# Optimization experiments

Measured on AMD Instinct MI355X. Metric: run time of the kernel, lower is better.

## Reference

```python
import jax, jax.numpy as jnp
import numpy as np

N_NODES = 50000
N_EDGES = 800000
D = 128        # input_dim == output_dim
D_EDGE = 64    # edge_attr_size
Z_DIM = 2 * D + D_EDGE  # 320


def setup_inputs() -> dict:
    key = jax.random.key(0)
    k1, k2, k3, k4, k5 = jax.random.split(key, 5)
    x = jax.random.normal(k1, (N_NODES, D), dtype=jnp.float32)
    edge_index = jax.random.randint(k2, (2, N_EDGES), 0, N_NODES, dtype=jnp.int64)
    edge_attr = jax.random.normal(k3, (N_EDGES, D_EDGE), dtype=jnp.float32)
    scale = 1.0 / np.sqrt(Z_DIM)
    W_f = jax.random.normal(k4, (Z_DIM, D), dtype=jnp.float32) * scale
    W_s = jax.random.normal(k5, (Z_DIM, D), dtype=jnp.float32) * scale
    b_f = jnp.zeros((D,), dtype=jnp.float32)
    b_s = jnp.zeros((D,), dtype=jnp.float32)
    return {"x": x, "edge_index": edge_index, "edge_attr": edge_attr,
            "W_f": W_f, "b_f": b_f, "W_s": W_s, "b_s": b_s}


def reference(x, edge_index, edge_attr, W_f, b_f, W_s, b_s):
    # Dropout(p=0.0) is identity in inference.
    src = edge_index[0]  # j (message source)
    dst = edge_index[1]  # i (message target)
    # z_e = [x_i, x_j, e_ij]  -> [E, 2D + D_edge]
    z = jnp.concatenate([x[dst], x[src], edge_attr], axis=-1)
    # CGConv message: sigmoid(lin_f(z)) * softplus(lin_s(z))
    msg = jax.nn.sigmoid(z @ W_f + b_f) * jax.nn.softplus(z @ W_s + b_s)
    # scatter-add aggregation + residual
    out = jax.ops.segment_sum(msg, dst, num_segments=x.shape[0]) + x
    # use_activation=True -> ReLU
    return jax.nn.relu(out)
```

## Files before the change

kernel.cpp:

```cpp
#include <hip/hip_runtime.h>
#include <hip/hip_bf16.h>

#define E_TOTAL   800000
#define NN        50000
#define DD        128
#define DE        64
#define ZDIM      320
#define KE        192
#define MT        64
#define NBS       196

typedef short bf16x8 __attribute__((ext_vector_type(8)));
typedef float f32x4  __attribute__((ext_vector_type(4)));

__device__ __forceinline__ unsigned short f2bf(float f) {
    union { float f; unsigned int u; } v; v.f = f;
    unsigned int u = v.u;
    return (unsigned short)((u + 0x7fffu + ((u >> 16) & 1u)) >> 16);
}

__device__ __forceinline__ float bf2f(unsigned short h) {
    union { unsigned u; float f; } v; v.u = ((unsigned)h) << 16; return v.f;
}

__device__ __forceinline__ unsigned pkbf2(float a, float b) {
    __hip_bfloat162 h = __float22bfloat162_rn(make_float2(a, b));
    unsigned u; __builtin_memcpy(&u, &h, 4); return u;
}

__device__ __forceinline__ uint2 pkbf4(float4 v) {
    uint2 r; r.x = pkbf2(v.x, v.y); r.y = pkbf2(v.z, v.w); return r;
}

__device__ __forceinline__ float fast_rcp(float x) {
#if __has_builtin(__builtin_amdgcn_rcpf)
    return __builtin_amdgcn_rcpf(x);
#else
    return 1.0f / x;
#endif
}


__global__ void scan_part(const int* __restrict__ counts, int* __restrict__ partial) {
    __shared__ int red[256];
    int t = threadIdx.x, k = blockIdx.x * 256 + t;
    red[t] = (k < NN) ? counts[k] : 0;
    __syncthreads();
    for (int d = 128; d > 0; d >>= 1) {
        if (t < d) red[t] += red[t + d];
        __syncthreads();
    }
    if (t == 0) partial[blockIdx.x] = red[0];
}

__global__ void scan_top(int* __restrict__ partial) {
    __shared__ int s[256];
    int t = threadIdx.x;
    int v = (t < NBS) ? partial[t] : 0;
    s[t] = v; __syncthreads();
    for (int d = 1; d < 256; d <<= 1) {
        int a = (t >= d) ? s[t - d] : 0;
        __syncthreads();
        s[t] += a;
        __syncthreads();
    }
    if (t < NBS) partial[t] = s[t] - v;
}

__global__ void scan_final(const int* __restrict__ counts,
                           const int* __restrict__ partial,
                           int* __restrict__ cursor) {
    __shared__ int s[256];
    int t = threadIdx.x, k = blockIdx.x * 256 + t;
    int v = (k < NN) ? counts[k] : 0;
    s[t] = v; __syncthreads();
    for (int d = 1; d < 256; d <<= 1) {
        int a = (t >= d) ? s[t - d] : 0;
        __syncthreads();
        s[t] += a;
        __syncthreads();
    }
    if (k < NN) cursor[k] = partial[blockIdx.x] + s[t] - v;
}

__global__ void scatter_kernel(const int* __restrict__ ei, int* __restrict__ cursor,
                               uint2* __restrict__ spak2) {
    int e = blockIdx.x * 256 + threadIdx.x;
    if (e < E_TOTAL) {
        int d = ei[E_TOTAL + e];
        int pos = atomicAdd(&cursor[d], 1);
        uint2 p; p.x = ((unsigned)d << 16) | (unsigned)ei[e]; p.y = (unsigned)e;
        spak2[pos] = p;
    }
}


__global__ void prep_kernel2(const float* __restrict__ x,
                             const int* __restrict__ ei,
                             const float* __restrict__ W_f,
                             const float* __restrict__ W_s,
                             unsigned short* __restrict__ WtE,
                             unsigned short* __restrict__ WtN,
                             int* __restrict__ counts,
                             float* __restrict__ out) {
    int id = blockIdx.x * 256 + threadIdx.x;
    ((float4*)out)[id] = ((const float4*)x)[id];
    if (id < E_TOTAL) atomicAdd(&counts[ei[E_TOTAL + id]], 1);
    if (id < 256 * DE) {
        int n = id >> 6, k = id & 63;
        int ok = 2 * DD + k;
        float wv = (n < DD) ? W_f[ok * DD + n] : W_s[ok * DD + (n - DD)];
        WtE[id] = f2bf(wv);
    } else if (id < 256 * DE + 2 * 256 * DD) {
        int id2 = id - 256 * DE;
        int part = id2 >> 15;
        int r = id2 & 32767;
        int n = r >> 7, k = r & 127;
        int ok = part * DD + k;
        float wv = (n < DD) ? W_f[ok * DD + n] : W_s[ok * DD + (n - DD)];
        WtN[id2] = f2bf(wv);
    }
}

__global__ __launch_bounds__(256, 4)
void node_kernel2(const float* __restrict__ x,
                  const unsigned short* __restrict__ WtN,
                  const float* __restrict__ bf_, const float* __restrict__ bs_,
                  unsigned short* __restrict__ nodeP) {
    __shared__ unsigned short A_lds[MT * DD];
    const int t = threadIdx.x;
    const int m_off = blockIdx.x * MT;
    const int part = blockIdx.y;
    const int lane = t & 63, w = t >> 6, l15 = lane & 15, quad = lane >> 4;

    #pragma unroll
    for (int it = 0; it < 8; ++it) {
        int idx = it * 256 + t;
        int e = idx >> 5, kq = idx & 31;
        int row = m_off + e; if (row >= NN) row = NN - 1;
        float4 v = ((const float4*)(x + (size_t)row * DD))[kq];
        int g = kq >> 1;
        int col = ((g & ~7) | ((g & 7) ^ (e & 7))) * 8 + (kq & 1) * 4;
        *((uint2*)&A_lds[e * DD + col]) = pkbf4(v);
    }

    f32x4 acc[4][4] = {};
    const int nt0 = 2 * w;
    const unsigned short* Bp[4];
    #pragma unroll
    for (int u = 0; u < 4; ++u) {
        int nt = nt0 + ((u < 2) ? u : (6 + u));
        Bp[u] = WtN + (size_t)part * (256 * DD) + (size_t)(nt * 16 + l15) * DD + quad * 8;
    }
    __syncthreads();

    #pragma unroll
    for (int ks = 0; ks < 4; ++ks) {
        bf16x8 af[4], bfr[4];
        #pragma unroll
        for (int i = 0; i < 4; ++i) {
            int m = i * 16 + l15;
            int g = 4 * ks + quad;
            int col = ((g & ~7) | ((g & 7) ^ (l15 & 7))) * 8;
            af[i] = *((const bf16x8*)&A_lds[m * DD + col]);
        }
        #pragma unroll
        for (int u = 0; u < 4; ++u)
            bfr[u] = *((const bf16x8*)(Bp[u] + ks * 32));
        #pragma unroll
        for (int i = 0; i < 4; ++i)
            #pragma unroll
            for (int u = 0; u < 4; ++u)
                acc[i][u] = __builtin_amdgcn_mfma_f32_16x16x32_bf16(
                    af[i], bfr[u], acc[i][u], 0, 0, 0);
    }

    const int c0 = 32 * w + l15, c1 = c0 + 16;
    const float bf0 = part ? 0.f : bf_[c0], bs0 = part ? 0.f : bs_[c0];
    const float bf1 = part ? 0.f : bf_[c1], bs1 = part ? 0.f : bs_[c1];
    #pragma unroll
    for (int i = 0; i < 4; ++i)
        #pragma unroll
        for (int j = 0; j < 4; ++j) {
            int e = i * 16 + quad * 4 + j;
            int row = m_off + e;
            if (row < NN) {
                uint2 pk;
                pk.x = pkbf2(acc[i][0][j] + bf0, acc[i][1][j] + bf1);
                pk.y = pkbf2(acc[i][2][j] + bs0, acc[i][3][j] + bs1);
                *((uint2*)(nodeP + (size_t)row * 512 + part * 256 + w * 64 + l15 * 4)) = pk;
            }
        }
}

#define PS_LOAD(PS, I)                                                          \
    _Pragma("unroll")                                                           \
    for (int j = 0; j < 4; ++j)                                                 \
        PS[j] = *((const uint2*)(npS + (size_t)src_lds[(I) * 16 + quad * 4 + j] * 512));

#define PS_PROC(PS, I)                                                          \
    _Pragma("unroll")                                                           \
    for (int j = 0; j < 4; ++j) {                                               \
        int e = (I) * 16 + quad * 4 + j;                                        \
        int dd = dst_lds[e];                                                    \
        if (dd != d) {                                                          \
            if (d >= 0) {                                                       \
                atomicAdd(out + (size_t)d * DD + c0, s0);                       \
                atomicAdd(out + (size_t)d * DD + c1, s1);                       \
            }                                                                   \
            d = dd; s0 = 0.f; s1 = 0.f;                                         \
            uint2 pk = *((const uint2*)(nodeP + (size_t)d * 512 + np_off));     \
            nf0 = bf2f((unsigned short)(pk.x & 0xffffu));                       \
            nf1 = bf2f((unsigned short)(pk.x >> 16));                           \
            ns0 = bf2f((unsigned short)(pk.y & 0xffffu));                       \
            ns1 = bf2f((unsigned short)(pk.y >> 16));                           \
        }                                                                       \
        uint2 pp = PS[j];                                                       \
        float f0  = acc[(I)][0][j] + nf0 + bf2f((unsigned short)(pp.x & 0xffffu)); \
        float f1  = acc[(I)][1][j] + nf1 + bf2f((unsigned short)(pp.x >> 16));  \
        float sg0 = acc[(I)][2][j] + ns0 + bf2f((unsigned short)(pp.y & 0xffffu)); \
        float sg1 = acc[(I)][3][j] + ns1 + bf2f((unsigned short)(pp.y >> 16));  \
        s0 += fast_rcp(1.f + __expf(-f0)) *                                     \
              (fmaxf(sg0, 0.f) + __logf(1.f + __expf(-fabsf(sg0))));            \
        s1 += fast_rcp(1.f + __expf(-f1)) *                                     \
              (fmaxf(sg1, 0.f) + __logf(1.f + __expf(-fabsf(sg1))));            \
    }

__global__ __launch_bounds__(256, 4)
void edge_kernel2(const float* __restrict__ ea,
                  const unsigned short* __restrict__ WtE,
                  const unsigned short* __restrict__ nodeP,
                  float* __restrict__ out,
                  const uint2* __restrict__ spak2) {
    __shared__ unsigned short A_lds[MT * DE];
    __shared__ int dst_lds[MT];
    __shared__ int src_lds[MT];
    __shared__ int eid_lds[MT];

    const int t = threadIdx.x;
    const int m_off = blockIdx.x * MT;
    const int lane = t & 63, w = t >> 6, l15 = lane & 15, quad = lane >> 4;

    if (t < MT) {
        uint2 p = spak2[m_off + t];
        dst_lds[t] = (int)(p.x >> 16);
        src_lds[t] = (int)(p.x & 0xffffu);
        eid_lds[t] = (int)p.y;
    }
    __syncthreads();

    #pragma unroll
    for (int it = 0; it < 4; ++it) {
        int idx = it * 256 + t;
        int e = idx >> 4, kq = idx & 15;
        float4 v = ((const float4*)(ea + (size_t)eid_lds[e] * DE))[kq];
        int g = kq >> 1;
        int col = ((g & 7) ^ (e & 7)) * 8 + (kq & 1) * 4;
        *((uint2*)&A_lds[e * DE + col]) = pkbf4(v);
    }

    f32x4 acc[4][4] = {};
    const int nt0 = 2 * w;
    const unsigned short* Bp[4];
    #pragma unroll
    for (int u = 0; u < 4; ++u) {
        int nt = nt0 + ((u < 2) ? u : (6 + u));
        Bp[u] = WtE + (size_t)(nt * 16 + l15) * DE + quad * 8;
    }
    __syncthreads();

    #pragma unroll
    for (int ks = 0; ks < 2; ++ks) {
        bf16x8 af[4], bfr[4];
        #pragma unroll
        for (int i = 0; i < 4; ++i) {
            int m = i * 16 + l15;
            int g = 4 * ks + quad;
            int col = ((g & 7) ^ (l15 & 7)) * 8;
            af[i] = *((const bf16x8*)&A_lds[m * DE + col]);
        }
        #pragma unroll
        for (int u = 0; u < 4; ++u)
            bfr[u] = *((const bf16x8*)(Bp[u] + ks * 32));
        #pragma unroll
        for (int i = 0; i < 4; ++i)
            #pragma unroll
            for (int u = 0; u < 4; ++u)
                acc[i][u] = __builtin_amdgcn_mfma_f32_16x16x32_bf16(
                    af[i], bfr[u], acc[i][u], 0, 0, 0);
    }

    const int c0 = 32 * w + l15, c1 = c0 + 16;
    const int np_off = w * 64 + l15 * 4;
    const unsigned short* npS = nodeP + 256 + np_off;

    int d = -1;
    float s0 = 0.f, s1 = 0.f, nf0 = 0.f, ns0 = 0.f, nf1 = 0.f, ns1 = 0.f;
    uint2 psA[4], psB[4];
    PS_LOAD(psA, 0)
    PS_LOAD(psB, 1)
    PS_PROC(psA, 0)
    PS_LOAD(psA, 2)
    PS_PROC(psB, 1)
    PS_LOAD(psB, 3)
    PS_PROC(psA, 2)
    PS_PROC(psB, 3)
    atomicAdd(out + (size_t)d * DD + c0, s0);
    atomicAdd(out + (size_t)d * DD + c1, s1);
}


__global__ void prep_kernel(const float* __restrict__ x,
                            const int* __restrict__ ei,
                            const float* __restrict__ W_f,
                            const float* __restrict__ W_s,
                            unsigned short* __restrict__ WtE,
                            unsigned short* __restrict__ WtN,
                            int* __restrict__ counts,
                            float* __restrict__ out) {
    int id = blockIdx.x * 256 + threadIdx.x;
    ((float4*)out)[id] = ((const float4*)x)[id];
    if (id < E_TOTAL) atomicAdd(&counts[ei[E_TOTAL + id]], 1);
    if (id < 256 * KE) {
        int n = id / KE, k = id - n * KE;
        int ok = 128 + k;
        float wv = (n < DD) ? W_f[ok * DD + n] : W_s[ok * DD + (n - DD)];
        WtE[id] = f2bf(wv);
    } else if (id < 256 * KE + 256 * DD) {
        int id2 = id - 256 * KE;
        int n = id2 / DD, k = id2 - n * DD;
        float wv = (n < DD) ? W_f[k * DD + n] : W_s[k * DD + (n - DD)];
        WtN[id2] = f2bf(wv);
    }
}

__global__ __launch_bounds__(256, 4)
void node_kernel(const float* __restrict__ x,
                 const unsigned short* __restrict__ WtN,
                 const float* __restrict__ bf_, const float* __restrict__ bs_,
                 unsigned short* __restrict__ nodeP) {
    __shared__ unsigned short A_lds[MT * DD];
    const int t = threadIdx.x;
    const int m_off = blockIdx.x * MT;
    const int lane = t & 63, w = t >> 6, l15 = lane & 15, quad = lane >> 4;

    #pragma unroll
    for (int it = 0; it < 8; ++it) {
        int idx = it * 256 + t;
        int e = idx >> 5, kq = idx & 31;
        int row = m_off + e; if (row >= NN) row = NN - 1;
        float4 v = ((const float4*)(x + (size_t)row * DD))[kq];
        int g = kq >> 1;
        int col = ((g & ~7) | ((g & 7) ^ (e & 7))) * 8 + (kq & 1) * 4;
        *((uint2*)&A_lds[e * DD + col]) = pkbf4(v);
    }

    f32x4 acc[4][4] = {};
    const int nt0 = 2 * w;
    const unsigned short* Bp[4];
    #pragma unroll
    for (int u = 0; u < 4; ++u) {
        int nt = nt0 + ((u < 2) ? u : (6 + u));
        Bp[u] = WtN + (size_t)(nt * 16 + l15) * DD + quad * 8;
    }
    __syncthreads();

    #pragma unroll
    for (int ks = 0; ks < 4; ++ks) {
        bf16x8 af[4], bfr[4];
        #pragma unroll
        for (int i = 0; i < 4; ++i) {
            int m = i * 16 + l15;
            int g = 4 * ks + quad;
            int col = ((g & ~7) | ((g & 7) ^ (l15 & 7))) * 8;
            af[i] = *((const bf16x8*)&A_lds[m * DD + col]);
        }
        #pragma unroll
        for (int u = 0; u < 4; ++u)
            bfr[u] = *((const bf16x8*)(Bp[u] + ks * 32));
        #pragma unroll
        for (int i = 0; i < 4; ++i)
            #pragma unroll
            for (int u = 0; u < 4; ++u)
                acc[i][u] = __builtin_amdgcn_mfma_f32_16x16x32_bf16(
                    af[i], bfr[u], acc[i][u], 0, 0, 0);
    }

    const int c0 = 32 * w + l15, c1 = c0 + 16;
    const float bf0 = bf_[c0], bs0 = bs_[c0], bf1 = bf_[c1], bs1 = bs_[c1];
    #pragma unroll
    for (int i = 0; i < 4; ++i)
        #pragma unroll
        for (int j = 0; j < 4; ++j) {
            int e = i * 16 + quad * 4 + j;
            int row = m_off + e;
            if (row < NN) {
                uint2 pk;
                pk.x = pkbf2(acc[i][0][j] + bf0, acc[i][1][j] + bf1);
                pk.y = pkbf2(acc[i][2][j] + bs0, acc[i][3][j] + bs1);
                *((uint2*)(nodeP + (size_t)row * 256 + w * 64 + l15 * 4)) = pk;
            }
        }
}

__global__ __launch_bounds__(256, 4)
void edge_kernel(const float* __restrict__ x,
                 const float* __restrict__ ea,
                 const unsigned short* __restrict__ WtE,
                 const unsigned short* __restrict__ nodeP,
                 float* __restrict__ out,
                 const uint2* __restrict__ spak2) {
    __shared__ unsigned short A_lds[MT * KE];
    __shared__ int dst_lds[MT];
    __shared__ int src_lds[MT];
    __shared__ int eid_lds[MT];

    const int t = threadIdx.x;
    const int m_off = blockIdx.x * MT;
    const int lane = t & 63, w = t >> 6, l15 = lane & 15, quad = lane >> 4;

    if (t < MT) {
        uint2 p = spak2[m_off + t];
        dst_lds[t] = (int)(p.x >> 16);
        src_lds[t] = (int)(p.x & 0xffffu);
        eid_lds[t] = (int)p.y;
    }
    __syncthreads();

    #pragma unroll
    for (int it = 0; it < 4; ++it) {
        int idx = it * 256 + t;
        int e = idx >> 4, kq = idx & 15;
        float4 v = ((const float4*)(ea + (size_t)eid_lds[e] * DE))[kq];
        int g = 16 + (kq >> 1);
        int col = ((g & ~7) | ((g & 7) ^ (e & 7))) * 8 + (kq & 1) * 4;
        *((uint2*)&A_lds[e * KE + col]) = pkbf4(v);
    }
    #pragma unroll
    for (int it = 0; it < 8; ++it) {
        int idx = it * 256 + t;
        int e = idx >> 5, kq = idx & 31;
        float4 v = ((const float4*)(x + (size_t)src_lds[e] * DD))[kq];
        int g = kq >> 1;
        int col = ((g & ~7) | ((g & 7) ^ (e & 7))) * 8 + (kq & 1) * 4;
        *((uint2*)&A_lds[e * KE + col]) = pkbf4(v);
    }

    f32x4 acc[4][4] = {};
    const int nt0 = 2 * w;
    const unsigned short* Bp[4];
    #pragma unroll
    for (int u = 0; u < 4; ++u) {
        int nt = nt0 + ((u < 2) ? u : (6 + u));
        Bp[u] = WtE + (size_t)(nt * 16 + l15) * KE + quad * 8;
    }
    __syncthreads();

    #pragma unroll
    for (int ks = 0; ks < 6; ++ks) {
        bf16x8 af[4], bfr[4];
        #pragma unroll
        for (int i = 0; i < 4; ++i) {
            int m = i * 16 + l15;
            int g = 4 * ks + quad;
            int col = ((g & ~7) | ((g & 7) ^ (l15 & 7))) * 8;
            af[i] = *((const bf16x8*)&A_lds[m * KE + col]);
        }
        #pragma unroll
        for (int u = 0; u < 4; ++u)
            bfr[u] = *((const bf16x8*)(Bp[u] + ks * 32));
        #pragma unroll
        for (int i = 0; i < 4; ++i)
            #pragma unroll
            for (int u = 0; u < 4; ++u)
                acc[i][u] = __builtin_amdgcn_mfma_f32_16x16x32_bf16(
                    af[i], bfr[u], acc[i][u], 0, 0, 0);
    }

    const int c0 = 32 * w + l15, c1 = c0 + 16;
    const int np_off = w * 64 + l15 * 4;

    int d = -1;
    float s0 = 0.f, s1 = 0.f, nf0 = 0.f, ns0 = 0.f, nf1 = 0.f, ns1 = 0.f;
    #pragma unroll
    for (int i = 0; i < 4; ++i)
        #pragma unroll
        for (int j = 0; j < 4; ++j) {
            int e = i * 16 + quad * 4 + j;
            int dd = dst_lds[e];
            if (dd != d) {
                if (d >= 0) {
                    atomicAdd(out + (size_t)d * DD + c0, s0);
                    atomicAdd(out + (size_t)d * DD + c1, s1);
                }
                d = dd; s0 = 0.f; s1 = 0.f;
                uint2 pk = *((const uint2*)(nodeP + (size_t)d * 256 + np_off));
                nf0 = bf2f((unsigned short)(pk.x & 0xffffu));
                nf1 = bf2f((unsigned short)(pk.x >> 16));
                ns0 = bf2f((unsigned short)(pk.y & 0xffffu));
                ns1 = bf2f((unsigned short)(pk.y >> 16));
            }
            float f0  = acc[i][0][j] + nf0;
            float sg0 = acc[i][2][j] + ns0;
            s0 += fast_rcp(1.f + __expf(-f0)) *
                  (fmaxf(sg0, 0.f) + __logf(1.f + __expf(-fabsf(sg0))));
            float f1  = acc[i][1][j] + nf1;
            float sg1 = acc[i][3][j] + ns1;
            s1 += fast_rcp(1.f + __expf(-f1)) *
                  (fmaxf(sg1, 0.f) + __logf(1.f + __expf(-fabsf(sg1))));
        }
    atomicAdd(out + (size_t)d * DD + c0, s0);
    atomicAdd(out + (size_t)d * DD + c1, s1);
}

__global__ void relu_kernel(float* __restrict__ out) {
    int id = blockIdx.x * 256 + threadIdx.x;
    if (id < NN * DD / 4) {
        float4 v = ((float4*)out)[id];
        v.x = fmaxf(v.x, 0.0f); v.y = fmaxf(v.y, 0.0f);
        v.z = fmaxf(v.z, 0.0f); v.w = fmaxf(v.w, 0.0f);
        ((float4*)out)[id] = v;
    }
}


__global__ void prep_fb(const float* __restrict__ x,
                        const float* __restrict__ W_f,
                        const float* __restrict__ W_s,
                        unsigned short* __restrict__ Wt,
                        float* __restrict__ out) {
    int id = blockIdx.x * 256 + threadIdx.x;
    if (id < NN * DD / 4)
        ((float4*)out)[id] = ((const float4*)x)[id];
    if (id < 2 * DD * ZDIM) {
        int n = id / ZDIM, k = id - n * ZDIM;
        float wv = (n < DD) ? W_f[k * DD + n] : W_s[k * DD + (n - DD)];
        Wt[n * ZDIM + k] = f2bf(wv);
    }
}

__global__ __launch_bounds__(256, 3)
void edge_fb(const float* __restrict__ x,
             const int* __restrict__ ei,
             const float* __restrict__ ea,
             const unsigned short* __restrict__ Wt,
             const float* __restrict__ bf_,
             const float* __restrict__ bs_,
             float* __restrict__ out) {
    __shared__ unsigned short A_lds[MT * ZDIM];
    __shared__ int dst_lds[MT];
    __shared__ int src_lds[MT];

    const int t = threadIdx.x;
    const int m_off = blockIdx.x * MT;
    const int lane = t & 63, w = t >> 6, l15 = lane & 15, quad = lane >> 4;

    if (t < MT) dst_lds[t] = ei[E_TOTAL + m_off + t];
    else if (t < 2 * MT) src_lds[t - MT] = ei[m_off + (t - MT)];
    __syncthreads();

    #pragma unroll
    for (int it = 0; it < 4; ++it) {
        int idx = it * 256 + t;
        int e = idx >> 4, kq = idx & 15;
        float4 v = ((const float4*)(ea + (size_t)(m_off + e) * DE))[kq];
        int g = 32 + (kq >> 1);
        int col = ((g & ~7) | ((g & 7) ^ (e & 7))) * 8 + (kq & 1) * 4;
        *((uint2*)&A_lds[e * ZDIM + col]) = pkbf4(v);
    }
    #pragma unroll
    for (int it = 0; it < 8; ++it) {
        int idx = it * 256 + t;
        int e = idx >> 5, kq = idx & 31;
        float4 v = ((const float4*)(x + (size_t)dst_lds[e] * DD))[kq];
        int g = kq >> 1;
        int col = ((g & ~7) | ((g & 7) ^ (e & 7))) * 8 + (kq & 1) * 4;
        *((uint2*)&A_lds[e * ZDIM + col]) = pkbf4(v);
    }
    #pragma unroll
    for (int it = 0; it < 8; ++it) {
        int idx = it * 256 + t;
        int e = idx >> 5, kq = idx & 31;
        float4 v = ((const float4*)(x + (size_t)src_lds[e] * DD))[kq];
        int g = 16 + (kq >> 1);
        int col = ((g & ~7) | ((g & 7) ^ (e & 7))) * 8 + (kq & 1) * 4;
        *((uint2*)&A_lds[e * ZDIM + col]) = pkbf4(v);
    }

    f32x4 acc[4][4] = {};
    const int nt0 = 2 * w;
    const unsigned short* Bp[4];
    #pragma unroll
    for (int u = 0; u < 4; ++u) {
        int nt = nt0 + ((u < 2) ? u : (6 + u));
        Bp[u] = Wt + (size_t)(nt * 16 + l15) * ZDIM + quad * 8;
    }
    __syncthreads();

    #pragma unroll
    for (int ks = 0; ks < 10; ++ks) {
        bf16x8 af[4], bfr[4];
        #pragma unroll
        for (int i = 0; i < 4; ++i) {
            int m = i * 16 + l15;
            int g = 4 * ks + quad;
            int col = ((g & ~7) | ((g & 7) ^ (l15 & 7))) * 8;
            af[i] = *((const bf16x8*)&A_lds[m * ZDIM + col]);
        }
        #pragma unroll
        for (int u = 0; u < 4; ++u)
            bfr[u] = *((const bf16x8*)(Bp[u] + ks * 32));
        #pragma unroll
        for (int i = 0; i < 4; ++i)
            #pragma unroll
            for (int u = 0; u < 4; ++u)
                acc[i][u] = __builtin_amdgcn_mfma_f32_16x16x32_bf16(
                    af[i], bfr[u], acc[i][u], 0, 0, 0);
    }

    const int c0 = 32 * w + l15, c1 = c0 + 16;
    const float bf0 = bf_[c0], bs0 = bs_[c0], bf1 = bf_[c1], bs1 = bs_[c1];
    #pragma unroll
    for (int i = 0; i < 4; ++i)
        #pragma unroll
        for (int j = 0; j < 4; ++j) {
            int e = i * 16 + quad * 4 + j;
            float* op = out + (size_t)dst_lds[e] * DD;
            float f0 = acc[i][0][j] + bf0;
            float sg0 = acc[i][2][j] + bs0;
            atomicAdd(op + c0, fast_rcp(1.f + __expf(-f0)) *
                (fmaxf(sg0, 0.f) + __logf(1.f + __expf(-fabsf(sg0)))));
            float f1 = acc[i][1][j] + bf1;
            float sg1 = acc[i][3][j] + bs1;
            atomicAdd(op + c1, fast_rcp(1.f + __expf(-f1)) *
                (fmaxf(sg1, 0.f) + __logf(1.f + __expf(-fabsf(sg1)))));
        }
}


extern "C" void kernel_launch(void* const* d_in, const int* in_sizes, int n_in,
                              void* d_out, int out_size, void* d_ws, size_t ws_size,
                              hipStream_t stream) {
    (void)in_sizes; (void)n_in; (void)out_size;
    const float* x   = (const float*)d_in[0];
    const int*   ei  = (const int*)d_in[1];
    const float* ea  = (const float*)d_in[2];
    const float* W_f = (const float*)d_in[3];
    const float* b_f = (const float*)d_in[4];
    const float* W_s = (const float*)d_in[5];
    const float* b_s = (const float*)d_in[6];
    float* out = (float*)d_out;

    char* ws = (char*)d_ws;
    const size_t WS_NEED2 = 58164864;
    const size_t WS_NEED1 = 32564864;

    if (ws_size >= WS_NEED2) {
        unsigned short* WtE2   = (unsigned short*)ws;
        unsigned short* WtN2   = (unsigned short*)(ws + 32768);
        int*            counts = (int*)(ws + 163840);
        int*            cursor = (int*)(ws + 363840);
        int*            partial= (int*)(ws + 563840);
        uint2*          spak2  = (uint2*)(ws + 564864);
        unsigned short* nodeP  = (unsigned short*)(ws + 6964864);

        hipMemsetAsync(counts, 0, NN * sizeof(int), stream);
        prep_kernel2<<<NN * DD / 4 / 256, 256, 0, stream>>>(
            x, ei, W_f, W_s, WtE2, WtN2, counts, out);
        scan_part<<<NBS, 256, 0, stream>>>(counts, partial);
        scan_top<<<1, 256, 0, stream>>>(partial);
        scan_final<<<NBS, 256, 0, stream>>>(counts, partial, cursor);
        scatter_kernel<<<(E_TOTAL + 255) / 256, 256, 0, stream>>>(ei, cursor, spak2);
        dim3 ng((NN + MT - 1) / MT, 2);
        node_kernel2<<<ng, 256, 0, stream>>>(x, WtN2, b_f, b_s, nodeP);
        edge_kernel2<<<E_TOTAL / MT, 256, 0, stream>>>(
            ea, WtE2, nodeP, out, spak2);
    } else if (ws_size >= WS_NEED1) {
        unsigned short* WtE    = (unsigned short*)ws;
        unsigned short* WtN    = (unsigned short*)(ws + 98304);
        int*            counts = (int*)(ws + 163840);
        int*            cursor = (int*)(ws + 363840);
        int*            partial= (int*)(ws + 563840);
        uint2*          spak2  = (uint2*)(ws + 564864);
        unsigned short* nodeP  = (unsigned short*)(ws + 6964864);

        hipMemsetAsync(counts, 0, NN * sizeof(int), stream);
        prep_kernel<<<NN * DD / 4 / 256, 256, 0, stream>>>(
            x, ei, W_f, W_s, WtE, WtN, counts, out);
        scan_part<<<NBS, 256, 0, stream>>>(counts, partial);
        scan_top<<<1, 256, 0, stream>>>(partial);
        scan_final<<<NBS, 256, 0, stream>>>(counts, partial, cursor);
        scatter_kernel<<<(E_TOTAL + 255) / 256, 256, 0, stream>>>(ei, cursor, spak2);
        node_kernel<<<(NN + MT - 1) / MT, 256, 0, stream>>>(x, WtN, b_f, b_s, nodeP);
        edge_kernel<<<E_TOTAL / MT, 256, 0, stream>>>(
            x, ea, WtE, nodeP, out, spak2);
    } else {
        unsigned short* Wt = (unsigned short*)ws;
        prep_fb<<<6250, 256, 0, stream>>>(x, W_f, W_s, Wt, out);
        edge_fb<<<E_TOTAL / MT, 256, 0, stream>>>(x, ei, ea, Wt, b_f, b_s, out);
    }

    relu_kernel<<<6250, 256, 0, stream>>>(out);
}
```

Before: 621.5 us.

## Prefetch all node-projection gathers before MFMA and loop both parts per node block

The edge kernel now issues every source-node gather (16 per thread) and the first destination-node gather per row group up front, together with the edge-attribute loads, before the MFMA section, so their global-memory latency overlaps with the matrix multiply. Launch bounds drop from 4 to 3 waves per SIMD to make room for the extra registers this holds. The node kernel now handles both weight halves in a loop inside one block, so the x tile is loaded and converted to bf16 once instead of twice, with half as many blocks launched. The cost is higher register pressure and lower occupancy in the edge kernel.

```diff
diff --git a/kernel.cpp b/kernel.cpp
--- a/kernel.cpp
+++ b/kernel.cpp
@@ -130,7 +130,6 @@
     __shared__ unsigned short A_lds[MT * DD];
     const int t = threadIdx.x;
     const int m_off = blockIdx.x * MT;
-    const int part = blockIdx.y;
     const int lane = t & 63, w = t >> 6, l15 = lane & 15, quad = lane >> 4;
 
     #pragma unroll
@@ -144,89 +143,64 @@
         *((uint2*)&A_lds[e * DD + col]) = pkbf4(v);
     }
 
-    f32x4 acc[4][4] = {};
+    const int c0 = 32 * w + l15, c1 = c0 + 16;
+    const float bfc0 = bf_[c0], bsc0 = bs_[c0];
+    const float bfc1 = bf_[c1], bsc1 = bs_[c1];
     const int nt0 = 2 * w;
-    const unsigned short* Bp[4];
-    #pragma unroll
-    for (int u = 0; u < 4; ++u) {
-        int nt = nt0 + ((u < 2) ? u : (6 + u));
-        Bp[u] = WtN + (size_t)part * (256 * DD) + (size_t)(nt * 16 + l15) * DD + quad * 8;
-    }
-    __syncthreads();
-
-    #pragma unroll
-    for (int ks = 0; ks < 4; ++ks) {
-        bf16x8 af[4], bfr[4];
-        #pragma unroll
-        for (int i = 0; i < 4; ++i) {
-            int m = i * 16 + l15;
-            int g = 4 * ks + quad;
-            int col = ((g & ~7) | ((g & 7) ^ (l15 & 7))) * 8;
-            af[i] = *((const bf16x8*)&A_lds[m * DD + col]);
-        }
-        #pragma unroll
-        for (int u = 0; u < 4; ++u)
-            bfr[u] = *((const bf16x8*)(Bp[u] + ks * 32));
+    __syncthreads();
+
+    #pragma unroll 1
+    for (int part = 0; part < 2; ++part) {
+        f32x4 acc[4][4] = {};
+        const unsigned short* Bp[4];
+        #pragma unroll
+        for (int u = 0; u < 4; ++u) {
+            int nt = nt0 + ((u < 2) ? u : (6 + u));
+            Bp[u] = WtN + (size_t)part * (256 * DD) +
+                    (size_t)(nt * 16 + l15) * DD + quad * 8;
+        }
+
+        #pragma unroll
+        for (int ks = 0; ks < 4; ++ks) {
+            bf16x8 af[4], bfr[4];
+            #pragma unroll
+            for (int i = 0; i < 4; ++i) {
+                int m = i * 16 + l15;
+                int g = 4 * ks + quad;
+                int col = ((g & ~7) | ((g & 7) ^ (l15 & 7))) * 8;
+                af[i] = *((const bf16x8*)&A_lds[m * DD + col]);
+            }
+            #pragma unroll
+            for (int u = 0; u < 4; ++u)
+                bfr[u] = *((const bf16x8*)(Bp[u] + ks * 32));
+            #pragma unroll
+            for (int i = 0; i < 4; ++i)
+                #pragma unroll
+                for (int u = 0; u < 4; ++u)
+                    acc[i][u] = __builtin_amdgcn_mfma_f32_16x16x32_bf16(
+                        af[i], bfr[u], acc[i][u], 0, 0, 0);
+        }
+
+        const float bf0 = part ? 0.f : bfc0, bs0 = part ? 0.f : bsc0;
+        const float bf1 = part ? 0.f : bfc1, bs1 = part ? 0.f : bsc1;
         #pragma unroll
         for (int i = 0; i < 4; ++i)
             #pragma unroll
-            for (int u = 0; u < 4; ++u)
-                acc[i][u] = __builtin_amdgcn_mfma_f32_16x16x32_bf16(
-                    af[i], bfr[u], acc[i][u], 0, 0, 0);
-    }
-
-    const int c0 = 32 * w + l15, c1 = c0 + 16;
-    const float bf0 = part ? 0.f : bf_[c0], bs0 = part ? 0.f : bs_[c0];
-    const float bf1 = part ? 0.f : bf_[c1], bs1 = part ? 0.f : bs_[c1];
-    #pragma unroll
-    for (int i = 0; i < 4; ++i)
-        #pragma unroll
-        for (int j = 0; j < 4; ++j) {
-            int e = i * 16 + quad * 4 + j;
-            int row = m_off + e;
-            if (row < NN) {
-                uint2 pk;
-                pk.x = pkbf2(acc[i][0][j] + bf0, acc[i][1][j] + bf1);
-                pk.y = pkbf2(acc[i][2][j] + bs0, acc[i][3][j] + bs1);
-                *((uint2*)(nodeP + (size_t)row * 512 + part * 256 + w * 64 + l15 * 4)) = pk;
+            for (int j = 0; j < 4; ++j) {
+                int e = i * 16 + quad * 4 + j;
+                int row = m_off + e;
+                if (row < NN) {
+                    uint2 pk;
+                    pk.x = pkbf2(acc[i][0][j] + bf0, acc[i][1][j] + bf1);
+                    pk.y = pkbf2(acc[i][2][j] + bs0, acc[i][3][j] + bs1);
+                    *((uint2*)(nodeP + (size_t)row * 512 + part * 256 +
+                               w * 64 + l15 * 4)) = pk;
+                }
             }
-        }
-}
-
-#define PS_LOAD(PS, I)                                                          \
-    _Pragma("unroll")                                                           \
-    for (int j = 0; j < 4; ++j)                                                 \
-        PS[j] = *((const uint2*)(npS + (size_t)src_lds[(I) * 16 + quad * 4 + j] * 512));
-
-#define PS_PROC(PS, I)                                                          \
-    _Pragma("unroll")                                                           \
-    for (int j = 0; j < 4; ++j) {                                               \
-        int e = (I) * 16 + quad * 4 + j;                                        \
-        int dd = dst_lds[e];                                                    \
-        if (dd != d) {                                                          \
-            if (d >= 0) {                                                       \
-                atomicAdd(out + (size_t)d * DD + c0, s0);                       \
-                atomicAdd(out + (size_t)d * DD + c1, s1);                       \
-            }                                                                   \
-            d = dd; s0 = 0.f; s1 = 0.f;                                         \
-            uint2 pk = *((const uint2*)(nodeP + (size_t)d * 512 + np_off));     \
-            nf0 = bf2f((unsigned short)(pk.x & 0xffffu));                       \
-            nf1 = bf2f((unsigned short)(pk.x >> 16));                           \
-            ns0 = bf2f((unsigned short)(pk.y & 0xffffu));                       \
-            ns1 = bf2f((unsigned short)(pk.y >> 16));                           \
-        }                                                                       \
-        uint2 pp = PS[j];                                                       \
-        float f0  = acc[(I)][0][j] + nf0 + bf2f((unsigned short)(pp.x & 0xffffu)); \
-        float f1  = acc[(I)][1][j] + nf1 + bf2f((unsigned short)(pp.x >> 16));  \
-        float sg0 = acc[(I)][2][j] + ns0 + bf2f((unsigned short)(pp.y & 0xffffu)); \
-        float sg1 = acc[(I)][3][j] + ns1 + bf2f((unsigned short)(pp.y >> 16));  \
-        s0 += fast_rcp(1.f + __expf(-f0)) *                                     \
-              (fmaxf(sg0, 0.f) + __logf(1.f + __expf(-fabsf(sg0))));            \
-        s1 += fast_rcp(1.f + __expf(-f1)) *                                     \
-              (fmaxf(sg1, 0.f) + __logf(1.f + __expf(-fabsf(sg1))));            \
-    }
-
-__global__ __launch_bounds__(256, 4)
+    }
+}
+
+__global__ __launch_bounds__(256, 3)
 void edge_kernel2(const float* __restrict__ ea,
                   const unsigned short* __restrict__ WtE,
                   const unsigned short* __restrict__ nodeP,
@@ -249,14 +223,34 @@
     }
     __syncthreads();
 
+    const int c0 = 32 * w + l15, c1 = c0 + 16;
+    const int np_off = w * 64 + l15 * 4;
+    const unsigned short* npS = nodeP + 256 + np_off;
+
+    float4 va[4];
     #pragma unroll
     for (int it = 0; it < 4; ++it) {
         int idx = it * 256 + t;
+        int e = idx >> 4;
+        va[it] = ((const float4*)(ea + (size_t)eid_lds[e] * DE))[idx & 15];
+    }
+    uint2 ps[16], pd[4];
+    #pragma unroll
+    for (int i = 0; i < 4; ++i) {
+        #pragma unroll
+        for (int j = 0; j < 4; ++j)
+            ps[i * 4 + j] = *((const uint2*)(npS +
+                (size_t)src_lds[i * 16 + quad * 4 + j] * 512));
+        pd[i] = *((const uint2*)(nodeP +
+                (size_t)dst_lds[i * 16 + quad * 4] * 512 + np_off));
+    }
+    #pragma unroll
+    for (int it = 0; it < 4; ++it) {
+        int idx = it * 256 + t;
         int e = idx >> 4, kq = idx & 15;
-        float4 v = ((const float4*)(ea + (size_t)eid_lds[e] * DE))[kq];
         int g = kq >> 1;
         int col = ((g & 7) ^ (e & 7)) * 8 + (kq & 1) * 4;
-        *((uint2*)&A_lds[e * DE + col]) = pkbf4(v);
+        *((uint2*)&A_lds[e * DE + col]) = pkbf4(va[it]);
     }
 
     f32x4 acc[4][4] = {};
@@ -290,21 +284,38 @@
                     af[i], bfr[u], acc[i][u], 0, 0, 0);
     }
 
-    const int c0 = 32 * w + l15, c1 = c0 + 16;
-    const int np_off = w * 64 + l15 * 4;
-    const unsigned short* npS = nodeP + 256 + np_off;
-
     int d = -1;
     float s0 = 0.f, s1 = 0.f, nf0 = 0.f, ns0 = 0.f, nf1 = 0.f, ns1 = 0.f;
-    uint2 psA[4], psB[4];
-    PS_LOAD(psA, 0)
-    PS_LOAD(psB, 1)
-    PS_PROC(psA, 0)
-    PS_LOAD(psA, 2)
-    PS_PROC(psB, 1)
-    PS_LOAD(psB, 3)
-    PS_PROC(psA, 2)
-    PS_PROC(psB, 3)
+    #pragma unroll
+    for (int i = 0; i < 4; ++i)
+        #pragma unroll
+        for (int j = 0; j < 4; ++j) {
+            int e = i * 16 + quad * 4 + j;
+            int dd = dst_lds[e];
+            if (dd != d) {
+                if (d >= 0) {
+                    atomicAdd(out + (size_t)d * DD + c0, s0);
+                    atomicAdd(out + (size_t)d * DD + c1, s1);
+                }
+                d = dd; s0 = 0.f; s1 = 0.f;
+                uint2 pk;
+                if (j == 0) pk = pd[i];
+                else pk = *((const uint2*)(nodeP + (size_t)dd * 512 + np_off));
+                nf0 = bf2f((unsigned short)(pk.x & 0xffffu));
+                nf1 = bf2f((unsigned short)(pk.x >> 16));
+                ns0 = bf2f((unsigned short)(pk.y & 0xffffu));
+                ns1 = bf2f((unsigned short)(pk.y >> 16));
+            }
+            uint2 pp = ps[i * 4 + j];
+            float f0  = acc[i][0][j] + nf0 + bf2f((unsigned short)(pp.x & 0xffffu));
+            float f1  = acc[i][1][j] + nf1 + bf2f((unsigned short)(pp.x >> 16));
+            float sg0 = acc[i][2][j] + ns0 + bf2f((unsigned short)(pp.y & 0xffffu));
+            float sg1 = acc[i][3][j] + ns1 + bf2f((unsigned short)(pp.y >> 16));
+            s0 += fast_rcp(1.f + __expf(-f0)) *
+                  (fmaxf(sg0, 0.f) + __logf(1.f + __expf(-fabsf(sg0))));
+            s1 += fast_rcp(1.f + __expf(-f1)) *
+                  (fmaxf(sg1, 0.f) + __logf(1.f + __expf(-fabsf(sg1))));
+        }
     atomicAdd(out + (size_t)d * DD + c0, s0);
     atomicAdd(out + (size_t)d * DD + c1, s1);
 }
@@ -671,8 +682,7 @@
         scan_top<<<1, 256, 0, stream>>>(partial);
         scan_final<<<NBS, 256, 0, stream>>>(counts, partial, cursor);
         scatter_kernel<<<(E_TOTAL + 255) / 256, 256, 0, stream>>>(ei, cursor, spak2);
-        dim3 ng((NN + MT - 1) / MT, 2);
-        node_kernel2<<<ng, 256, 0, stream>>>(x, WtN2, b_f, b_s, nodeP);
+        node_kernel2<<<(NN + MT - 1) / MT, 256, 0, stream>>>(x, WtN2, b_f, b_s, nodeP);
         edge_kernel2<<<E_TOTAL / MT, 256, 0, stream>>>(
             ea, WtE2, nodeP, out, spak2);
     } else if (ws_size >= WS_NEED1) {
```

Result: slower. 671.9 us (+8.1%).
